# Performance work log

Measured on AMD Instinct MI355X. Metric: run time of the kernel, lower is better.

The kernel has to match this reference:

```python
import jax, jax.numpy as jnp
import numpy as np

B, T, P, H, LAT = 64, 256, 128, 512, 128


def _run_lstm(x, Wih, Whh, b, h0, c0):
    """Single unidirectional LSTM layer, PyTorch gate order (i,f,g,o).
    x: (B,T,in) -> outputs (B,T,H), final h (B,H)."""
    xW = jnp.einsum('bti,gi->btg', x, Wih) + b  # precompute input projection (B,T,4H)

    def step(carry, xw_t):
        h, c = carry
        g = xw_t + h @ Whh.T
        i, f, gg, o = jnp.split(g, 4, axis=-1)
        c = jax.nn.sigmoid(f) * c + jax.nn.sigmoid(i) * jnp.tanh(gg)
        h = jax.nn.sigmoid(o) * jnp.tanh(c)
        return (h, c), h

    (hT, cT), hs = jax.lax.scan(step, (h0, c0), jnp.swapaxes(xW, 0, 1))
    return jnp.swapaxes(hs, 0, 1), hT


def setup_inputs() -> dict:
    key = jax.random.key(0)
    ks = iter(jax.random.split(key, 40))
    rn = lambda shape, s=0.05: jax.random.normal(next(ks), shape, jnp.float32) * s
    inp = {
        'x': (jax.random.uniform(next(ks), (B, T, P)) < 0.1).astype(jnp.float32),
        'e0f_Wih': rn((4 * H, P)), 'e0f_Whh': rn((4 * H, H)), 'e0f_b': jnp.zeros((4 * H,), jnp.float32),
        'e0b_Wih': rn((4 * H, P)), 'e0b_Whh': rn((4 * H, H)), 'e0b_b': jnp.zeros((4 * H,), jnp.float32),
        'e1f_Wih': rn((4 * H, 2 * H)), 'e1f_Whh': rn((4 * H, H)), 'e1f_b': jnp.zeros((4 * H,), jnp.float32),
        'e1b_Wih': rn((4 * H, 2 * H)), 'e1b_Whh': rn((4 * H, H)), 'e1b_b': jnp.zeros((4 * H,), jnp.float32),
        'enc_fc_W': rn((LAT, 2 * H)), 'enc_fc_b': jnp.zeros((LAT,), jnp.float32),
        'dec_fc_W': rn((H, LAT)), 'dec_fc_b': jnp.zeros((H,), jnp.float32),
        'start_token': rn((1, 1, P), 0.1),
        'd0_Wih': rn((4 * H, P)), 'd0_Whh': rn((4 * H, H)), 'd0_b': jnp.zeros((4 * H,), jnp.float32),
        'd1_Wih': rn((4 * H, H)), 'd1_Whh': rn((4 * H, H)), 'd1_b': jnp.zeros((4 * H,), jnp.float32),
        'out_W': rn((P, H)), 'out_b': jnp.zeros((P,), jnp.float32),
        'teacher_forcing_ratio': 1,
    }
    return inp


def reference(x, e0f_Wih, e0f_Whh, e0f_b, e0b_Wih, e0b_Whh, e0b_b,
              e1f_Wih, e1f_Whh, e1f_b, e1b_Wih, e1b_Whh, e1b_b,
              enc_fc_W, enc_fc_b, dec_fc_W, dec_fc_b, start_token,
              d0_Wih, d0_Whh, d0_b, d1_Wih, d1_Whh, d1_b, out_W, out_b,
              teacher_forcing_ratio):
    b = x.shape[0]
    z0 = jnp.zeros((b, H), x.dtype)
    # ---- encoder: 2-layer bidirectional LSTM ----
    f0, _ = _run_lstm(x, e0f_Wih, e0f_Whh, e0f_b, z0, z0)
    r0, _ = _run_lstm(x[:, ::-1], e0b_Wih, e0b_Whh, e0b_b, z0, z0)
    l0 = jnp.concatenate([f0, r0[:, ::-1]], axis=-1)  # (B,T,2H)
    _, h_fwd = _run_lstm(l0, e1f_Wih, e1f_Whh, e1f_b, z0, z0)
    _, h_bwd = _run_lstm(l0[:, ::-1], e1b_Wih, e1b_Whh, e1b_b, z0, z0)
    z = jnp.concatenate([h_fwd, h_bwd], axis=-1) @ enc_fc_W.T + enc_fc_b  # (B,LAT)
    # ---- decoder: teacher-forced 2-layer LSTM ----
    h0d = z @ dec_fc_W.T + dec_fc_b  # (B,H), repeated for every layer
    xs = jnp.concatenate([jnp.broadcast_to(start_token, (b, 1, P)), x[:, :-1]], axis=1)
    o0, _ = _run_lstm(xs, d0_Wih, d0_Whh, d0_b, h0d, z0)
    o1, _ = _run_lstm(o0, d1_Wih, d1_Whh, d1_b, h0d, z0)
    x_hat = jax.nn.sigmoid(o1 @ out_W.T + out_b)  # (B,T,P)
    return x_hat, z
```

## Files before the change

### kernel.cpp

```cpp
#include <hip/hip_runtime.h>
#include <stdint.h>


typedef unsigned short u16;
typedef unsigned int u32;
typedef float f32x4 __attribute__((ext_vector_type(4)));
typedef __bf16 bf16x8 __attribute__((ext_vector_type(8)));
typedef unsigned int u32x4 __attribute__((ext_vector_type(4)));

#define AT_LD(p) __hip_atomic_load((p), __ATOMIC_RELAXED, __HIP_MEMORY_SCOPE_AGENT)
#define AT_ST(p, v) __hip_atomic_store((p), (v), __ATOMIC_RELAXED, __HIP_MEMORY_SCOPE_AGENT)

__device__ __forceinline__ u16 f2bf(float f) {
  u32 u = __builtin_bit_cast(u32, f);
  u += 0x7FFFu + ((u >> 16) & 1u);
  return (u16)(u >> 16);
}
__device__ __forceinline__ float bf2f(u16 h) {
  return __builtin_bit_cast(float, (u32)h << 16);
}
__device__ __forceinline__ bf16x8 ld8(const u16* p) {
  u32x4 v = *(const u32x4*)p;
  return __builtin_bit_cast(bf16x8, v);
}
__device__ __forceinline__ float sigf(float x) { return 1.f / (1.f + __expf(-x)); }
__device__ __forceinline__ float tanhx(float x) {
  x = fminf(fmaxf(x, -15.f), 15.f);
  float e = __expf(2.f * x);
  return (e - 1.f) / (e + 1.f);
}

__global__ void k_prep_x(const float* __restrict__ x, const float* __restrict__ st,
                         u16* __restrict__ Ax, u16* __restrict__ Axs, int n) {
  int i = blockIdx.x * 256 + threadIdx.x;
  if (i >= n) return;
  Ax[i] = f2bf(x[i]);
  int col = i & 127;
  int t = (i >> 7) & 255;
  float v = (t == 0) ? st[col] : x[i - 128];
  Axs[i] = f2bf(v);
}

struct CvtJobs {
  const float* src[13];
  u16* dst[13];
  int off[14];
};
__global__ void k_cvt_all(CvtJobs j, int total) {
  int i = blockIdx.x * 256 + threadIdx.x;
  if (i >= total) return;
  int a = 0;
#pragma unroll
  for (int k = 1; k < 13; ++k) a += (i >= j.off[k]) ? 1 : 0;
  int local = i - j.off[a];
  j.dst[a][local] = f2bf(j.src[a][local]);
}

__global__ __launch_bounds__(256) void k_gemm_bt(
    const u16* __restrict__ A, const u16* __restrict__ B, const float* __restrict__ bias,
    u16* __restrict__ Cb, float* __restrict__ Cf, int M, int N, int K, int sig) {
  __shared__ __align__(16) u16 As[128 * 64];
  __shared__ __align__(16) u16 Bs[128 * 64];
  const int m0 = blockIdx.x * 128, n0 = blockIdx.y * 128;
  const int tid = threadIdx.x, lane = tid & 63, wave = tid >> 6;
  const int wm = wave >> 1, wn = wave & 1;

  f32x4 acc[4][4];
#pragma unroll
  for (int i = 0; i < 4; ++i)
#pragma unroll
    for (int j = 0; j < 4; ++j) acc[i][j] = (f32x4){0.f, 0.f, 0.f, 0.f};

  const int nkt = K >> 6;
  for (int kt = 0; kt < nkt; ++kt) {
#pragma unroll
    for (int i = 0; i < 4; ++i) {
      int ch = tid + (i << 8);
      int row = ch >> 3, k8 = ch & 7;
      int dst = row * 128 + ((k8 * 16) ^ ((row & 7) << 4));
      u32x4 va = *(const u32x4*)(A + (size_t)(m0 + row) * K + kt * 64 + k8 * 8);
      *(u32x4*)((char*)As + dst) = va;
      u32x4 vb = *(const u32x4*)(B + (size_t)(n0 + row) * K + kt * 64 + k8 * 8);
      *(u32x4*)((char*)Bs + dst) = vb;
    }
    __syncthreads();
#pragma unroll
    for (int kk = 0; kk < 2; ++kk) {
      int kb = kk * 64 + ((lane >> 4) << 4);
      bf16x8 afr[4], bfr[4];
#pragma unroll
      for (int i = 0; i < 4; ++i) {
        int ra = wm * 64 + i * 16 + (lane & 15);
        afr[i] = ld8((const u16*)((const char*)As + ra * 128 + (kb ^ ((ra & 7) << 4))));
        int rb = wn * 64 + i * 16 + (lane & 15);
        bfr[i] = ld8((const u16*)((const char*)Bs + rb * 128 + (kb ^ ((rb & 7) << 4))));
      }
#pragma unroll
      for (int i = 0; i < 4; ++i)
#pragma unroll
        for (int j = 0; j < 4; ++j)
          acc[i][j] = __builtin_amdgcn_mfma_f32_16x16x32_bf16(afr[i], bfr[j], acc[i][j], 0, 0, 0);
    }
    __syncthreads();
  }
#pragma unroll
  for (int i = 0; i < 4; ++i) {
#pragma unroll
    for (int j = 0; j < 4; ++j) {
      int col = n0 + wn * 64 + j * 16 + (lane & 15);
      float bv = bias ? bias[col] : 0.f;
#pragma unroll
      for (int r = 0; r < 4; ++r) {
        int row = m0 + wm * 64 + i * 16 + ((lane >> 4) << 2) + r;
        float v = acc[i][j][r] + bv;
        if (sig) Cf[(size_t)row * N + col] = 1.f / (1.f + __expf(-v));
        else     Cb[(size_t)row * N + col] = f2bf(v);
      }
    }
  }
}

struct Rec3 {
  const u16* xW[8];
  const u16* Whh[8];
  const u16* Wih[8];
  const float* bias[8];
  const float* h0[8];
  u16* seq[8];
  float* hfin[8];
  u16* hxc[8];
  int prod[8];
  int seqstride[8]; int coloff[8]; int rev[8]; int hfinstride[8];
  int grp[8]; int fused[8]; int fullp[8];
  u32* tags;
};

__global__ __launch_bounds__(256, 1) void k_rec3(Rec3 p) {
  const int chain = blockIdx.x & 7;
  const int c = blockIdx.x >> 3;
  const int tid = threadIdx.x, lane = tid & 63, wave = tid >> 6;
  const int arow = lane & 15, kg = lane >> 4;
  const int g4 = arow & 3;
  const int h4 = arow >> 2;
  const int myrow = (kg << 2) + g4;
  const int mycol = (wave << 2) + h4;

  const u16* __restrict__ xW = p.xW[chain];
  const u16* __restrict__ Whh = p.Whh[chain];
  const u16* __restrict__ Wih = p.Wih[chain];
  const float* __restrict__ bias = p.bias[chain];
  const float* __restrict__ h0 = p.h0[chain];
  u16* seq = p.seq[chain];
  float* hfin = p.hfin[chain];
  u32* hx = (u32*)p.hxc[chain];
  const u32* hxp = (const u32*)p.hxc[p.prod[chain]];
  const int grp = p.grp[chain], rev = p.rev[chain];
  const int fused = p.fused[chain], fullp = p.fullp[chain];
  const int sstride = p.seqstride[chain], coloff = p.coloff[chain];
  const int hstride = p.hfinstride[chain];
  u32* myt = p.tags + chain * 128;
  const u32* pt = p.tags + p.prod[chain] * 128;

  __shared__ __align__(16) u16 Wlds[64][64][8];
  __shared__ __align__(16) u16 Xlds[64][64][8];
  __shared__ __align__(16) u16 hbufA[8192];
  __shared__ float bbuf[64];

  for (int e = tid; e < 4096; e += 256) {
    int n = e >> 6, k8 = e & 63;
    int grow = ((n & 3) << 9) + (c << 4) + (n >> 2);
    int ns = n ^ (k8 & 3);
    *(u32x4*)(&Wlds[k8][ns][0]) = *(const u32x4*)(Whh + (size_t)grow * 512 + k8 * 8);
    if (fused)
      *(u32x4*)(&Xlds[k8][ns][0]) = *(const u32x4*)(Wih + (size_t)grow * 512 + k8 * 8);
  }
  if (tid < 64) bbuf[tid] = fused ? bias[((tid & 3) << 9) + (c << 4) + (tid >> 2)] : 0.f;

  float creg = 0.f;

  {
    float hv = h0 ? h0[(size_t)(grp * 16 + myrow) * 512 + (c << 4) + mycol] : 0.f;
    u32 mypk = (u32)f2bf(hv);
    u32 part = (u32)__shfl_xor((int)mypk, 4);
    if ((h4 & 1) == 0)
      AT_ST(hx + ((size_t)0 * 32 + c) * 128 + (myrow << 3) + (mycol >> 1), mypk | (part << 16));
  }
  asm volatile("s_waitcnt vmcnt(0)" ::: "memory");
  if (lane == 0) AT_ST(myt + c * 4 + wave, 1u);
  __syncthreads();

  for (int t = 0; t < 256; ++t) {
    const int t_eff = rev ? 255 - t : t;
    const int slot = fullp ? t : (t & 3);
    const int slotn = fullp ? (t + 1) : ((t + 1) & 3);

    float xwv[4] = {0.f, 0.f, 0.f, 0.f};
    if (!fused) {
#pragma unroll
      for (int r = 0; r < 4; ++r) {
        int row = (kg << 2) + r;
        xwv[r] = bf2f(xW[((size_t)((grp * 16 + row) * 256 + t_eff)) * 2048 +
                         (g4 << 9) + (c << 4) + mycol]);
      }
    }
    if (wave == 0) {
      u32 to = (u32)(t + 1), tp = (u32)(t + 2);
      while (true) {
        int ok = (AT_LD(myt + lane) >= to) & (AT_LD(myt + 64 + lane) >= to);
        if (fused) ok &= (AT_LD(pt + lane) >= tp) & (AT_LD(pt + 64 + lane) >= tp);
        if (__all(ok)) break;
        __builtin_amdgcn_s_sleep(1);
      }
    }
    __syncthreads();

#pragma unroll
    for (int i = 0; i < 4; ++i) {
      int cid = tid + (i << 8);
      int row = cid >> 6, ch8 = cid & 63;
      const u32* src = hx + ((size_t)slot * 32 + (ch8 >> 1)) * 128 +
                       (row << 3) + ((ch8 & 1) << 2);
      u32x4 v;
      v.x = AT_LD(src + 0); v.y = AT_LD(src + 1);
      v.z = AT_LD(src + 2); v.w = AT_LD(src + 3);
      *(u32x4*)((char*)hbufA + row * 1024 + ((ch8 << 4) ^ ((row & 7) << 4))) = v;
    }
    bf16x8 xf[16];
    if (fused) {
#pragma unroll
      for (int kt = 0; kt < 16; ++kt) {
        const u32* hp = hxp + ((size_t)(t + 1) * 32 + 2 * kt + (kg >> 1)) * 128 +
                        (arow << 3) + ((kg & 1) << 2);
        u32x4 v;
        v.x = AT_LD(hp + 0); v.y = AT_LD(hp + 1);
        v.z = AT_LD(hp + 2); v.w = AT_LD(hp + 3);
        xf[kt] = __builtin_bit_cast(bf16x8, v);
      }
    }
    __syncthreads();

    bf16x8 af[16];
#pragma unroll
    for (int kt = 0; kt < 16; ++kt)
      af[kt] = ld8((const u16*)((const char*)hbufA + arow * 1024 +
                                ((kt * 64 + (kg << 4)) ^ ((arow & 7) << 4))));
    f32x4 ae = {0.f, 0.f, 0.f, 0.f}, ao = {0.f, 0.f, 0.f, 0.f};
    const int nswz = (wave << 4) + arow;
#pragma unroll
    for (int kt = 0; kt < 16; ++kt) {
      bf16x8 bw = ld8(&Wlds[(kt << 2) + kg][nswz ^ kg][0]);
      if (kt & 1) ao = __builtin_amdgcn_mfma_f32_16x16x32_bf16(af[kt], bw, ao, 0, 0, 0);
      else        ae = __builtin_amdgcn_mfma_f32_16x16x32_bf16(af[kt], bw, ae, 0, 0, 0);
      if (fused) {
        bf16x8 bx = ld8(&Xlds[(kt << 2) + kg][nswz ^ kg][0]);
        if (kt & 1) ae = __builtin_amdgcn_mfma_f32_16x16x32_bf16(xf[kt], bx, ae, 0, 0, 0);
        else        ao = __builtin_amdgcn_mfma_f32_16x16x32_bf16(xf[kt], bx, ao, 0, 0, 0);
      }
    }
    float bb = bbuf[nswz];
    float a0 = ae[0] + ao[0] + xwv[0] + bb;
    float a1 = ae[1] + ao[1] + xwv[1] + bb;
    float a2 = ae[2] + ao[2] + xwv[2] + bb;
    float a3 = ae[3] + ao[3] + xwv[3] + bb;

    float b0, b1, b2, b3;
    {
      float s0 = __shfl_xor(a0, 1), s1 = __shfl_xor(a1, 1);
      float s2 = __shfl_xor(a2, 1), s3 = __shfl_xor(a3, 1);
      bool j0 = (lane & 1) != 0;
      b0 = j0 ? s1 : a0;
      b1 = j0 ? a1 : s0;
      b2 = j0 ? s3 : a2;
      b3 = j0 ? a3 : s2;
    }
    float iv, fv, gv, ov;
    {
      float u0 = __shfl_xor(b0, 2), u1 = __shfl_xor(b1, 2);
      float u2 = __shfl_xor(b2, 2), u3 = __shfl_xor(b3, 2);
      bool j1 = (lane & 2) != 0;
      iv = j1 ? u2 : b0;
      fv = j1 ? u3 : b1;
      gv = j1 ? b2 : u0;
      ov = j1 ? b3 : u1;
    }
    float cc = sigf(fv) * creg + sigf(iv) * tanhx(gv);
    creg = cc;
    float hh = sigf(ov) * tanhx(cc);

    u32 mypk = (u32)f2bf(hh);
    u32 part = (u32)__shfl_xor((int)mypk, 4);
    u32 pk = mypk | (part << 16);
    bool evenh = ((h4 & 1) == 0);
    if (evenh)
      AT_ST(hx + ((size_t)slotn * 32 + c) * 128 + (myrow << 3) + (mycol >> 1), pk);
    asm volatile("s_waitcnt vmcnt(0)" ::: "memory");
    if (lane == 0) AT_ST(myt + c * 4 + wave, (u32)(t + 2));
    if (seq && evenh)
      *(u32*)(seq + ((size_t)((grp * 16 + myrow) * 256 + t_eff)) * sstride +
              coloff + (c << 4) + mycol) = pk;
    if (hfin && t == 255)
      hfin[(size_t)(grp * 16 + myrow) * hstride + (c << 4) + mycol] = hh;
  }
}

__global__ void k_enc_head(const float* __restrict__ hcat, const float* __restrict__ W,
                           const float* __restrict__ b, float* __restrict__ zws,
                           float* __restrict__ zout) {
  int bi = blockIdx.x, j = threadIdx.x;
  const float* h = hcat + bi * 1024;
  const float* w = W + j * 1024;
  float s = b[j];
  for (int k = 0; k < 1024; ++k) s += h[k] * w[k];
  zws[bi * 128 + j] = s;
  zout[bi * 128 + j] = s;
}

__global__ void k_dec_head(const float* __restrict__ z, const float* __restrict__ W,
                           const float* __restrict__ b, float* __restrict__ h0d) {
  int bi = blockIdx.x, j = threadIdx.x;
  const float* zz = z + bi * 128;
  const float* w = W + j * 128;
  float s = b[j];
  for (int k = 0; k < 128; ++k) s += zz[k] * w[k];
  h0d[bi * 512 + j] = s;
}

extern "C" void kernel_launch(void* const* d_in, const int* in_sizes, int n_in,
                              void* d_out, int out_size, void* d_ws, size_t ws_size,
                              hipStream_t stream) {
  (void)in_sizes; (void)n_in; (void)out_size;
  const float* x        = (const float*)d_in[0];
  const float* e0f_Wih  = (const float*)d_in[1];
  const float* e0f_Whh  = (const float*)d_in[2];
  const float* e0f_b    = (const float*)d_in[3];
  const float* e0b_Wih  = (const float*)d_in[4];
  const float* e0b_Whh  = (const float*)d_in[5];
  const float* e0b_b    = (const float*)d_in[6];
  const float* e1f_Wih  = (const float*)d_in[7];
  const float* e1f_Whh  = (const float*)d_in[8];
  const float* e1f_b    = (const float*)d_in[9];
  const float* e1b_Wih  = (const float*)d_in[10];
  const float* e1b_Whh  = (const float*)d_in[11];
  const float* e1b_b    = (const float*)d_in[12];
  const float* enc_fc_W = (const float*)d_in[13];
  const float* enc_fc_b = (const float*)d_in[14];
  const float* dec_fc_W = (const float*)d_in[15];
  const float* dec_fc_b = (const float*)d_in[16];
  const float* start_tk = (const float*)d_in[17];
  const float* d0_Wih   = (const float*)d_in[18];
  const float* d0_Whh   = (const float*)d_in[19];
  const float* d0_b     = (const float*)d_in[20];
  const float* d1_Wih   = (const float*)d_in[21];
  const float* d1_Whh   = (const float*)d_in[22];
  const float* d1_b     = (const float*)d_in[23];
  const float* out_W    = (const float*)d_in[24];
  const float* out_b    = (const float*)d_in[25];

  uintptr_t base = (uintptr_t)d_ws;
  size_t off = 0;
  auto carve = [&](size_t bytes) -> void* {
    off = (off + 255) & ~(size_t)255;
    void* p = (void*)(base + off);
    off += bytes;
    return p;
  };
  u16* Ax     = (u16*)carve((size_t)2097152 * 2);
  u16* Axs    = (u16*)carve((size_t)2097152 * 2);
  u16* Wb_e0f = (u16*)carve((size_t)262144 * 2);
  u16* Wb_e0b = (u16*)carve((size_t)262144 * 2);
  u16* Wb_d0  = (u16*)carve((size_t)262144 * 2);
  u16* Wb_e1f = (u16*)carve((size_t)2097152 * 2);
  u16* Wb_e1b = (u16*)carve((size_t)2097152 * 2);
  u16* Wb_d1  = (u16*)carve((size_t)1048576 * 2);
  u16* Wb_out = (u16*)carve((size_t)65536 * 2);
  u16* Wh_e0f = (u16*)carve((size_t)1048576 * 2);
  u16* Wh_e0b = (u16*)carve((size_t)1048576 * 2);
  u16* Wh_e1f = (u16*)carve((size_t)1048576 * 2);
  u16* Wh_e1b = (u16*)carve((size_t)1048576 * 2);
  u16* Wh_d0  = (u16*)carve((size_t)1048576 * 2);
  u16* Wh_d1  = (u16*)carve((size_t)1048576 * 2);
  u16* slot0  = (u16*)carve((size_t)16384 * 2048 * 2);
  u16* slot1  = (u16*)carve((size_t)16384 * 2048 * 2);
  u16* l0     = (u16*)carve((size_t)33619968);
  u16* hxring = (u16*)carve((size_t)524288);
  float* hcat = (float*)carve((size_t)65536 * 4);
  float* zws  = (float*)carve((size_t)8192 * 4);
  float* h0d  = (float*)carve((size_t)32768 * 4);
  u32* tags0  = (u32*)carve(4096);
  u32* tags1  = (u32*)carve(4096);
  u32* tags2  = (u32*)carve(4096);
  if (off > ws_size) return;

  u16* o1     = l0;
  u16* hxprod = l0 + 8388608;

  (void)hipMemsetAsync(tags0, 0, 12288, stream);

  k_prep_x<<<8192, 256, 0, stream>>>(x, start_tk, Ax, Axs, 2097152);
  {
    CvtJobs j{};
    const float* s[13] = {e0f_Wih, e0b_Wih, d0_Wih, e1f_Wih, e1b_Wih, d1_Wih, out_W,
                          e0f_Whh, e0b_Whh, e1f_Whh, e1b_Whh, d0_Whh, d1_Whh};
    u16* d[13] = {Wb_e0f, Wb_e0b, Wb_d0, Wb_e1f, Wb_e1b, Wb_d1, Wb_out,
                  Wh_e0f, Wh_e0b, Wh_e1f, Wh_e1b, Wh_d0, Wh_d1};
    int n[13] = {262144, 262144, 262144, 2097152, 2097152, 1048576, 65536,
                 1048576, 1048576, 1048576, 1048576, 1048576, 1048576};
    int acc = 0;
    for (int k = 0; k < 13; ++k) { j.src[k] = s[k]; j.dst[k] = d[k]; j.off[k] = acc; acc += n[k]; }
    j.off[13] = acc;
    k_cvt_all<<<(acc + 255) / 256, 256, 0, stream>>>(j, acc);
  }

  k_gemm_bt<<<dim3(128, 16), 256, 0, stream>>>(Ax, Wb_e0f, e0f_b, slot0, nullptr, 16384, 2048, 128, 0);
  k_gemm_bt<<<dim3(128, 16), 256, 0, stream>>>(Ax, Wb_e0b, e0b_b, slot1, nullptr, 16384, 2048, 128, 0);
  {
    Rec3 r{};
    for (int ch = 0; ch < 8; ++ch) {
      int dir2 = ch >> 2, g = ch & 3;
      r.xW[ch] = dir2 ? slot1 : slot0;
      r.Whh[ch] = dir2 ? Wh_e0b : Wh_e0f;
      r.Wih[ch] = nullptr; r.bias[ch] = nullptr; r.h0[ch] = nullptr;
      r.seq[ch] = l0; r.seqstride[ch] = 1024; r.coloff[ch] = dir2 ? 512 : 0;
      r.rev[ch] = dir2; r.hfin[ch] = nullptr; r.hfinstride[ch] = 0;
      r.grp[ch] = g; r.fused[ch] = 0; r.fullp[ch] = 0; r.prod[ch] = 0;
      r.hxc[ch] = hxring + (size_t)ch * 32768;
    }
    r.tags = tags0;
    k_rec3<<<256, 256, 0, stream>>>(r);
  }
  k_gemm_bt<<<dim3(128, 16), 256, 0, stream>>>(l0, Wb_e1f, e1f_b, slot0, nullptr, 16384, 2048, 1024, 0);
  k_gemm_bt<<<dim3(128, 16), 256, 0, stream>>>(l0, Wb_e1b, e1b_b, slot1, nullptr, 16384, 2048, 1024, 0);
  {
    Rec3 r{};
    for (int ch = 0; ch < 8; ++ch) {
      int dir2 = ch >> 2, g = ch & 3;
      r.xW[ch] = dir2 ? slot1 : slot0;
      r.Whh[ch] = dir2 ? Wh_e1b : Wh_e1f;
      r.Wih[ch] = nullptr; r.bias[ch] = nullptr; r.h0[ch] = nullptr;
      r.seq[ch] = nullptr; r.seqstride[ch] = 0; r.coloff[ch] = 0;
      r.rev[ch] = dir2; r.hfin[ch] = hcat + (dir2 ? 512 : 0); r.hfinstride[ch] = 1024;
      r.grp[ch] = g; r.fused[ch] = 0; r.fullp[ch] = 0; r.prod[ch] = 0;
      r.hxc[ch] = hxring + (size_t)ch * 32768;
    }
    r.tags = tags1;
    k_rec3<<<256, 256, 0, stream>>>(r);
  }
  k_enc_head<<<64, 128, 0, stream>>>(hcat, enc_fc_W, enc_fc_b, zws, ((float*)d_out) + 2097152);
  k_dec_head<<<64, 512, 0, stream>>>(zws, dec_fc_W, dec_fc_b, h0d);
  k_gemm_bt<<<dim3(128, 16), 256, 0, stream>>>(Axs, Wb_d0, d0_b, slot0, nullptr, 16384, 2048, 128, 0);
  {
    Rec3 r{};
    for (int ch = 0; ch < 4; ++ch) {
      r.xW[ch] = slot0;
      r.Whh[ch] = Wh_d0;
      r.Wih[ch] = nullptr; r.bias[ch] = nullptr; r.h0[ch] = h0d;
      r.seq[ch] = nullptr; r.seqstride[ch] = 0; r.coloff[ch] = 0;
      r.rev[ch] = 0; r.hfin[ch] = nullptr; r.hfinstride[ch] = 0;
      r.grp[ch] = ch; r.fused[ch] = 0; r.fullp[ch] = 1; r.prod[ch] = 0;
      r.hxc[ch] = hxprod + (size_t)ch * 2105344;
    }
    for (int ch = 4; ch < 8; ++ch) {
      r.xW[ch] = nullptr;
      r.Whh[ch] = Wh_d1;
      r.Wih[ch] = Wb_d1; r.bias[ch] = d1_b; r.h0[ch] = h0d;
      r.seq[ch] = o1; r.seqstride[ch] = 512; r.coloff[ch] = 0;
      r.rev[ch] = 0; r.hfin[ch] = nullptr; r.hfinstride[ch] = 0;
      r.grp[ch] = ch - 4; r.fused[ch] = 1; r.fullp[ch] = 0; r.prod[ch] = ch - 4;
      r.hxc[ch] = hxring + (size_t)ch * 32768;
    }
    r.tags = tags2;
    k_rec3<<<256, 256, 0, stream>>>(r);
  }
  k_gemm_bt<<<dim3(128, 1), 256, 0, stream>>>(o1, Wb_out, out_b, nullptr, (float*)d_out, 16384, 128, 512, 1);
}
```

Before: 5.689 ms.

## Embed timestep tags in 64-bit hidden-state words to replace separate flag polling

Each packed bf16 hidden-state pair is now stored as a 64-bit word whose upper half holds the timestep tag. Consumers poll the data words directly until every tag matches, which drops the separate tag array, the vmcnt wait before publishing the flag, and the second round-trip to reload the data. Producer hidden states for the fused decoder layer are staged through a shared-memory buffer instead of being loaded straight into registers, and the bias is held in a register instead of shared memory. The tag buffers are no longer zeroed between calls, so stale tags left in reused ring memory could match an expected timestep; the data traffic also doubles in size.

```diff
diff --git a/kernel.cpp b/kernel.cpp
--- a/kernel.cpp
+++ b/kernel.cpp
@@ -4,12 +4,13 @@
 
 typedef unsigned short u16;
 typedef unsigned int u32;
+typedef unsigned long long u64;
 typedef float f32x4 __attribute__((ext_vector_type(4)));
 typedef __bf16 bf16x8 __attribute__((ext_vector_type(8)));
 typedef unsigned int u32x4 __attribute__((ext_vector_type(4)));
 
-#define AT_LD(p) __hip_atomic_load((p), __ATOMIC_RELAXED, __HIP_MEMORY_SCOPE_AGENT)
-#define AT_ST(p, v) __hip_atomic_store((p), (v), __ATOMIC_RELAXED, __HIP_MEMORY_SCOPE_AGENT)
+#define AT_LD64(p) __hip_atomic_load((p), __ATOMIC_RELAXED, __HIP_MEMORY_SCOPE_AGENT)
+#define AT_ST64(p, v) __hip_atomic_store((p), (v), __ATOMIC_RELAXED, __HIP_MEMORY_SCOPE_AGENT)
 
 __device__ __forceinline__ u16 f2bf(float f) {
   u32 u = __builtin_bit_cast(u32, f);
@@ -120,7 +121,7 @@
   }
 }
 
-struct Rec3 {
+struct Rec4 {
   const u16* xW[8];
   const u16* Whh[8];
   const u16* Wih[8];
@@ -128,14 +129,13 @@
   const float* h0[8];
   u16* seq[8];
   float* hfin[8];
-  u16* hxc[8];
-  int prod[8];
+  u64* hx[8];
+  const u64* hxp[8];
   int seqstride[8]; int coloff[8]; int rev[8]; int hfinstride[8];
   int grp[8]; int fused[8]; int fullp[8];
-  u32* tags;
 };
 
-__global__ __launch_bounds__(256, 1) void k_rec3(Rec3 p) {
+__global__ __launch_bounds__(256, 1) void k_rec4(Rec4 p) {
   const int chain = blockIdx.x & 7;
   const int c = blockIdx.x >> 3;
   const int tid = threadIdx.x, lane = tid & 63, wave = tid >> 6;
@@ -152,29 +152,29 @@
   const float* __restrict__ h0 = p.h0[chain];
   u16* seq = p.seq[chain];
   float* hfin = p.hfin[chain];
-  u32* hx = (u32*)p.hxc[chain];
-  const u32* hxp = (const u32*)p.hxc[p.prod[chain]];
+  u64* hx = p.hx[chain];
+  const u64* hxp = p.hxp[chain];
   const int grp = p.grp[chain], rev = p.rev[chain];
   const int fused = p.fused[chain], fullp = p.fullp[chain];
   const int sstride = p.seqstride[chain], coloff = p.coloff[chain];
   const int hstride = p.hfinstride[chain];
-  u32* myt = p.tags + chain * 128;
-  const u32* pt = p.tags + p.prod[chain] * 128;
-
-  __shared__ __align__(16) u16 Wlds[64][64][8];
-  __shared__ __align__(16) u16 Xlds[64][64][8];
-  __shared__ __align__(16) u16 hbufA[8192];
-  __shared__ float bbuf[64];
+
+  __shared__ __align__(16) u16 LDSALL[81920];
+  u16* Wlds = LDSALL;
+  u16* Xlds = LDSALL + 32768;
+  char* hbufA = (char*)(LDSALL + 65536);
+  char* hbufX = (char*)(LDSALL + 73728);
 
   for (int e = tid; e < 4096; e += 256) {
     int n = e >> 6, k8 = e & 63;
     int grow = ((n & 3) << 9) + (c << 4) + (n >> 2);
     int ns = n ^ (k8 & 3);
-    *(u32x4*)(&Wlds[k8][ns][0]) = *(const u32x4*)(Whh + (size_t)grow * 512 + k8 * 8);
+    *(u32x4*)(Wlds + k8 * 512 + ns * 8) = *(const u32x4*)(Whh + (size_t)grow * 512 + k8 * 8);
     if (fused)
-      *(u32x4*)(&Xlds[k8][ns][0]) = *(const u32x4*)(Wih + (size_t)grow * 512 + k8 * 8);
-  }
-  if (tid < 64) bbuf[tid] = fused ? bias[((tid & 3) << 9) + (c << 4) + (tid >> 2)] : 0.f;
+      *(u32x4*)(Xlds + k8 * 512 + ns * 8) = *(const u32x4*)(Wih + (size_t)grow * 512 + k8 * 8);
+  }
+  const int nswz = (wave << 4) + arow;
+  const float breg = fused ? bias[((nswz & 3) << 9) + (c << 4) + (nswz >> 2)] : 0.f;
 
   float creg = 0.f;
 
@@ -183,16 +183,17 @@
     u32 mypk = (u32)f2bf(hv);
     u32 part = (u32)__shfl_xor((int)mypk, 4);
     if ((h4 & 1) == 0)
-      AT_ST(hx + ((size_t)0 * 32 + c) * 128 + (myrow << 3) + (mycol >> 1), mypk | (part << 16));
-  }
-  asm volatile("s_waitcnt vmcnt(0)" ::: "memory");
-  if (lane == 0) AT_ST(myt + c * 4 + wave, 1u);
-  __syncthreads();
+      AT_ST64(hx + (size_t)c * 128 + (myrow << 3) + (mycol >> 1),
+              ((u64)1 << 32) | (u64)(mypk | (part << 16)));
+  }
+
+  const int sc = tid >> 3;
+  const int r0 = (tid & 7) << 1;
 
   for (int t = 0; t < 256; ++t) {
     const int t_eff = rev ? 255 - t : t;
-    const int slot = fullp ? t : (t & 3);
-    const int slotn = fullp ? (t + 1) : ((t + 1) & 3);
+    const size_t slotbase = (size_t)(fullp ? t : (t & 3)) * 4096;
+    const size_t slotbn = (size_t)(fullp ? (t + 1) : ((t + 1) & 3)) * 4096;
 
     float xwv[4] = {0.f, 0.f, 0.f, 0.f};
     if (!fused) {
@@ -203,65 +204,83 @@
                          (g4 << 9) + (c << 4) + mycol]);
       }
     }
-    if (wave == 0) {
-      u32 to = (u32)(t + 1), tp = (u32)(t + 2);
+    __syncthreads();
+
+    {
+      const u64* src = hx + slotbase + (size_t)tid * 16;
+      const u32 expo = (u32)(t + 1);
+      u64 v[16];
       while (true) {
-        int ok = (AT_LD(myt + lane) >= to) & (AT_LD(myt + 64 + lane) >= to);
-        if (fused) ok &= (AT_LD(pt + lane) >= tp) & (AT_LD(pt + 64 + lane) >= tp);
+        int ok = 1;
+#pragma unroll
+        for (int i = 0; i < 16; ++i) {
+          v[i] = AT_LD64(src + i);
+          ok &= ((u32)(v[i] >> 32) == expo);
+        }
         if (__all(ok)) break;
         __builtin_amdgcn_s_sleep(1);
       }
+#pragma unroll
+      for (int j = 0; j < 2; ++j) {
+        int row = r0 + j;
+        char* rowb = hbufA + row * 1024;
+        u32x4 a = {(u32)v[j * 8 + 0], (u32)v[j * 8 + 1], (u32)v[j * 8 + 2], (u32)v[j * 8 + 3]};
+        u32x4 b = {(u32)v[j * 8 + 4], (u32)v[j * 8 + 5], (u32)v[j * 8 + 6], (u32)v[j * 8 + 7]};
+        int swz = (row & 7) << 4;
+        *(u32x4*)(rowb + ((sc * 32) ^ swz)) = a;
+        *(u32x4*)(rowb + ((sc * 32 + 16) ^ swz)) = b;
+      }
+    }
+    if (fused) {
+      const u64* src = hxp + (size_t)(t + 1) * 4096 + (size_t)tid * 16;
+      const u32 expo = (u32)(t + 2);
+      u64 v[16];
+      while (true) {
+        int ok = 1;
+#pragma unroll
+        for (int i = 0; i < 16; ++i) {
+          v[i] = AT_LD64(src + i);
+          ok &= ((u32)(v[i] >> 32) == expo);
+        }
+        if (__all(ok)) break;
+        __builtin_amdgcn_s_sleep(1);
+      }
+#pragma unroll
+      for (int j = 0; j < 2; ++j) {
+        int row = r0 + j;
+        char* rowb = hbufX + row * 1024;
+        u32x4 a = {(u32)v[j * 8 + 0], (u32)v[j * 8 + 1], (u32)v[j * 8 + 2], (u32)v[j * 8 + 3]};
+        u32x4 b = {(u32)v[j * 8 + 4], (u32)v[j * 8 + 5], (u32)v[j * 8 + 6], (u32)v[j * 8 + 7]};
+        int swz = (row & 7) << 4;
+        *(u32x4*)(rowb + ((sc * 32) ^ swz)) = a;
+        *(u32x4*)(rowb + ((sc * 32 + 16) ^ swz)) = b;
+      }
     }
     __syncthreads();
 
-#pragma unroll
-    for (int i = 0; i < 4; ++i) {
-      int cid = tid + (i << 8);
-      int row = cid >> 6, ch8 = cid & 63;
-      const u32* src = hx + ((size_t)slot * 32 + (ch8 >> 1)) * 128 +
-                       (row << 3) + ((ch8 & 1) << 2);
-      u32x4 v;
-      v.x = AT_LD(src + 0); v.y = AT_LD(src + 1);
-      v.z = AT_LD(src + 2); v.w = AT_LD(src + 3);
-      *(u32x4*)((char*)hbufA + row * 1024 + ((ch8 << 4) ^ ((row & 7) << 4))) = v;
-    }
-    bf16x8 xf[16];
-    if (fused) {
-#pragma unroll
-      for (int kt = 0; kt < 16; ++kt) {
-        const u32* hp = hxp + ((size_t)(t + 1) * 32 + 2 * kt + (kg >> 1)) * 128 +
-                        (arow << 3) + ((kg & 1) << 2);
-        u32x4 v;
-        v.x = AT_LD(hp + 0); v.y = AT_LD(hp + 1);
-        v.z = AT_LD(hp + 2); v.w = AT_LD(hp + 3);
-        xf[kt] = __builtin_bit_cast(bf16x8, v);
-      }
-    }
-    __syncthreads();
-
     bf16x8 af[16];
 #pragma unroll
     for (int kt = 0; kt < 16; ++kt)
-      af[kt] = ld8((const u16*)((const char*)hbufA + arow * 1024 +
+      af[kt] = ld8((const u16*)(hbufA + arow * 1024 +
                                 ((kt * 64 + (kg << 4)) ^ ((arow & 7) << 4))));
     f32x4 ae = {0.f, 0.f, 0.f, 0.f}, ao = {0.f, 0.f, 0.f, 0.f};
-    const int nswz = (wave << 4) + arow;
 #pragma unroll
     for (int kt = 0; kt < 16; ++kt) {
-      bf16x8 bw = ld8(&Wlds[(kt << 2) + kg][nswz ^ kg][0]);
+      bf16x8 bw = ld8(Wlds + ((kt << 2) + kg) * 512 + (nswz ^ kg) * 8);
       if (kt & 1) ao = __builtin_amdgcn_mfma_f32_16x16x32_bf16(af[kt], bw, ao, 0, 0, 0);
       else        ae = __builtin_amdgcn_mfma_f32_16x16x32_bf16(af[kt], bw, ae, 0, 0, 0);
       if (fused) {
-        bf16x8 bx = ld8(&Xlds[(kt << 2) + kg][nswz ^ kg][0]);
-        if (kt & 1) ae = __builtin_amdgcn_mfma_f32_16x16x32_bf16(xf[kt], bx, ae, 0, 0, 0);
-        else        ao = __builtin_amdgcn_mfma_f32_16x16x32_bf16(xf[kt], bx, ao, 0, 0, 0);
-      }
-    }
-    float bb = bbuf[nswz];
-    float a0 = ae[0] + ao[0] + xwv[0] + bb;
-    float a1 = ae[1] + ao[1] + xwv[1] + bb;
-    float a2 = ae[2] + ao[2] + xwv[2] + bb;
-    float a3 = ae[3] + ao[3] + xwv[3] + bb;
+        bf16x8 xg = ld8((const u16*)(hbufX + arow * 1024 +
+                                     ((kt * 64 + (kg << 4)) ^ ((arow & 7) << 4))));
+        bf16x8 bx = ld8(Xlds + ((kt << 2) + kg) * 512 + (nswz ^ kg) * 8);
+        if (kt & 1) ae = __builtin_amdgcn_mfma_f32_16x16x32_bf16(xg, bx, ae, 0, 0, 0);
+        else        ao = __builtin_amdgcn_mfma_f32_16x16x32_bf16(xg, bx, ao, 0, 0, 0);
+      }
+    }
+    float a0 = ae[0] + ao[0] + xwv[0] + breg;
+    float a1 = ae[1] + ao[1] + xwv[1] + breg;
+    float a2 = ae[2] + ao[2] + xwv[2] + breg;
+    float a3 = ae[3] + ao[3] + xwv[3] + breg;
 
     float b0, b1, b2, b3;
     {
@@ -292,9 +311,8 @@
     u32 pk = mypk | (part << 16);
     bool evenh = ((h4 & 1) == 0);
     if (evenh)
-      AT_ST(hx + ((size_t)slotn * 32 + c) * 128 + (myrow << 3) + (mycol >> 1), pk);
-    asm volatile("s_waitcnt vmcnt(0)" ::: "memory");
-    if (lane == 0) AT_ST(myt + c * 4 + wave, (u32)(t + 2));
+      AT_ST64(hx + slotbn + (size_t)c * 128 + (myrow << 3) + (mycol >> 1),
+              ((u64)(u32)(t + 2) << 32) | (u64)pk);
     if (seq && evenh)
       *(u32*)(seq + ((size_t)((grp * 16 + myrow) * 256 + t_eff)) * sstride +
               coloff + (c << 4) + mycol) = pk;
@@ -382,19 +400,16 @@
   u16* slot0  = (u16*)carve((size_t)16384 * 2048 * 2);
   u16* slot1  = (u16*)carve((size_t)16384 * 2048 * 2);
   u16* l0     = (u16*)carve((size_t)33619968);
-  u16* hxring = (u16*)carve((size_t)524288);
+  u64* hxE0   = (u64*)carve((size_t)131072 * 8);
+  u64* hxE1   = (u64*)carve((size_t)131072 * 8);
+  u64* hxD1   = (u64*)carve((size_t)65536 * 8);
   float* hcat = (float*)carve((size_t)65536 * 4);
   float* zws  = (float*)carve((size_t)8192 * 4);
   float* h0d  = (float*)carve((size_t)32768 * 4);
-  u32* tags0  = (u32*)carve(4096);
-  u32* tags1  = (u32*)carve(4096);
-  u32* tags2  = (u32*)carve(4096);
   if (off > ws_size) return;
 
-  u16* o1     = l0;
-  u16* hxprod = l0 + 8388608;
-
-  (void)hipMemsetAsync(tags0, 0, 12288, stream);
+  u16* o1   = l0;
+  u64* hxP  = (u64*)slot1;
 
   k_prep_x<<<8192, 256, 0, stream>>>(x, start_tk, Ax, Axs, 2097152);
   {
@@ -414,7 +429,7 @@
   k_gemm_bt<<<dim3(128, 16), 256, 0, stream>>>(Ax, Wb_e0f, e0f_b, slot0, nullptr, 16384, 2048, 128, 0);
   k_gemm_bt<<<dim3(128, 16), 256, 0, stream>>>(Ax, Wb_e0b, e0b_b, slot1, nullptr, 16384, 2048, 128, 0);
   {
-    Rec3 r{};
+    Rec4 r{};
     for (int ch = 0; ch < 8; ++ch) {
       int dir2 = ch >> 2, g = ch & 3;
       r.xW[ch] = dir2 ? slot1 : slot0;
@@ -422,16 +437,15 @@
       r.Wih[ch] = nullptr; r.bias[ch] = nullptr; r.h0[ch] = nullptr;
       r.seq[ch] = l0; r.seqstride[ch] = 1024; r.coloff[ch] = dir2 ? 512 : 0;
       r.rev[ch] = dir2; r.hfin[ch] = nullptr; r.hfinstride[ch] = 0;
-      r.grp[ch] = g; r.fused[ch] = 0; r.fullp[ch] = 0; r.prod[ch] = 0;
-      r.hxc[ch] = hxring + (size_t)ch * 32768;
-    }
-    r.tags = tags0;
-    k_rec3<<<256, 256, 0, stream>>>(r);
+      r.grp[ch] = g; r.fused[ch] = 0; r.fullp[ch] = 0;
+      r.hx[ch] = hxE0 + (size_t)ch * 16384; r.hxp[ch] = r.hx[ch];
+    }
+    k_rec4<<<256, 256, 0, stream>>>(r);
   }
   k_gemm_bt<<<dim3(128, 16), 256, 0, stream>>>(l0, Wb_e1f, e1f_b, slot0, nullptr, 16384, 2048, 1024, 0);
   k_gemm_bt<<<dim3(128, 16), 256, 0, stream>>>(l0, Wb_e1b, e1b_b, slot1, nullptr, 16384, 2048, 1024, 0);
   {
-    Rec3 r{};
+    Rec4 r{};
     for (int ch = 0; ch < 8; ++ch) {
       int dir2 = ch >> 2, g = ch & 3;
       r.xW[ch] = dir2 ? slot1 : slot0;
@@ -439,25 +453,24 @@
       r.Wih[ch] = nullptr; r.bias[ch] = nullptr; r.h0[ch] = nullptr;
       r.seq[ch] = nullptr; r.seqstride[ch] = 0; r.coloff[ch] = 0;
       r.rev[ch] = dir2; r.hfin[ch] = hcat + (dir2 ? 512 : 0); r.hfinstride[ch] = 1024;
-      r.grp[ch] = g; r.fused[ch] = 0; r.fullp[ch] = 0; r.prod[ch] = 0;
-      r.hxc[ch] = hxring + (size_t)ch * 32768;
-    }
-    r.tags = tags1;
-    k_rec3<<<256, 256, 0, stream>>>(r);
+      r.grp[ch] = g; r.fused[ch] = 0; r.fullp[ch] = 0;
+      r.hx[ch] = hxE1 + (size_t)ch * 16384; r.hxp[ch] = r.hx[ch];
+    }
+    k_rec4<<<256, 256, 0, stream>>>(r);
   }
   k_enc_head<<<64, 128, 0, stream>>>(hcat, enc_fc_W, enc_fc_b, zws, ((float*)d_out) + 2097152);
   k_dec_head<<<64, 512, 0, stream>>>(zws, dec_fc_W, dec_fc_b, h0d);
   k_gemm_bt<<<dim3(128, 16), 256, 0, stream>>>(Axs, Wb_d0, d0_b, slot0, nullptr, 16384, 2048, 128, 0);
   {
-    Rec3 r{};
+    Rec4 r{};
     for (int ch = 0; ch < 4; ++ch) {
       r.xW[ch] = slot0;
       r.Whh[ch] = Wh_d0;
       r.Wih[ch] = nullptr; r.bias[ch] = nullptr; r.h0[ch] = h0d;
       r.seq[ch] = nullptr; r.seqstride[ch] = 0; r.coloff[ch] = 0;
       r.rev[ch] = 0; r.hfin[ch] = nullptr; r.hfinstride[ch] = 0;
-      r.grp[ch] = ch; r.fused[ch] = 0; r.fullp[ch] = 1; r.prod[ch] = 0;
-      r.hxc[ch] = hxprod + (size_t)ch * 2105344;
+      r.grp[ch] = ch; r.fused[ch] = 0; r.fullp[ch] = 1;
+      r.hx[ch] = hxP + (size_t)ch * (257 * 4096); r.hxp[ch] = r.hx[ch];
     }
     for (int ch = 4; ch < 8; ++ch) {
       r.xW[ch] = nullptr;
@@ -465,11 +478,11 @@
       r.Wih[ch] = Wb_d1; r.bias[ch] = d1_b; r.h0[ch] = h0d;
       r.seq[ch] = o1; r.seqstride[ch] = 512; r.coloff[ch] = 0;
       r.rev[ch] = 0; r.hfin[ch] = nullptr; r.hfinstride[ch] = 0;
-      r.grp[ch] = ch - 4; r.fused[ch] = 1; r.fullp[ch] = 0; r.prod[ch] = ch - 4;
-      r.hxc[ch] = hxring + (size_t)ch * 32768;
-    }
-    r.tags = tags2;
-    k_rec3<<<256, 256, 0, stream>>>(r);
+      r.grp[ch] = ch - 4; r.fused[ch] = 1; r.fullp[ch] = 0;
+      r.hx[ch] = hxD1 + (size_t)(ch - 4) * 16384;
+      r.hxp[ch] = hxP + (size_t)(ch - 4) * (257 * 4096);
+    }
+    k_rec4<<<256, 256, 0, stream>>>(r);
   }
   k_gemm_bt<<<dim3(128, 1), 256, 0, stream>>>(o1, Wb_out, out_b, nullptr, (float*)d_out, 16384, 128, 512, 1);
 }
```

Result: slower. 7.637 ms (+34.2%).
